# Kernel optimization log

Hardware: AMD Instinct MI355X
Metric: run time of the kernel (lower is better)

Reference implementation:

```python
import jax, jax.numpy as jnp
import numpy as np
import math

B, L, D, H = 2, 2048, 1024, 16
HD = D // H

def setup_inputs() -> dict:
    key = jax.random.key(0)
    ks = jax.random.split(key, 8)
    s = 1.0 / math.sqrt(D)
    # causal additive mask: 0 on/below diagonal, -inf above
    causal = jnp.where(jnp.tril(jnp.ones((L, L), dtype=bool)), 0.0, -jnp.inf)
    causal = causal[None, None].astype(jnp.float32)  # [1,1,L,L]
    return {
        "Q": jax.random.normal(ks[0], (B, L, D), jnp.float32),
        "K": jax.random.normal(ks[1], (B, L, D), jnp.float32),
        "V": jax.random.normal(ks[2], (B, L, D), jnp.float32),
        "attn_mask": causal,
        "padding_mask": jnp.zeros((B, L), dtype=bool),
        "wq": jax.random.normal(ks[3], (D, D), jnp.float32) * s,
        "wk": jax.random.normal(ks[4], (D, D), jnp.float32) * s,
        "wv": jax.random.normal(ks[5], (D, D), jnp.float32) * s,
        "wout": jax.random.normal(ks[6], (D, D), jnp.float32) * s,
    }

def reference(Q, K, V, attn_mask, padding_mask, wq, wk, wv, wout):
    b, l, _ = Q.shape
    # projections (torch Linear: x @ W.T); weights sampled as [out,in]-like square
    def proj(x, w):
        return (x @ w.T).reshape(b, l, H, HD).transpose(0, 2, 1, 3)  # [B,H,L,hd]
    q = proj(Q, wq)
    k = proj(K, wk)
    v = proj(V, wv)
    scores = jnp.einsum("bhqd,bhkd->bhqk", q, k) / math.sqrt(HD)
    scores = scores + attn_mask
    scores = jnp.where(padding_mask[:, None, None, :], -jnp.inf, scores)
    weights = jax.nn.softmax(scores, axis=-1)
    ctx = jnp.einsum("bhqk,bhkd->bhqd", weights, v)
    ctx = ctx.transpose(0, 2, 1, 3).reshape(b, l, D)
    return ctx @ wout.T
```

## Files before the change

### kernel.cpp

```cpp
#include <hip/hip_runtime.h>
#include <stdint.h>
#include <stddef.h>

typedef __bf16 bf16_t;
typedef bf16_t bf16x4 __attribute__((ext_vector_type(4)));
typedef bf16_t bf16x8 __attribute__((ext_vector_type(8)));
typedef float f32x4 __attribute__((ext_vector_type(4)));

#define MFMA_BF16(A_, B_, C_) __builtin_amdgcn_mfma_f32_16x16x32_bf16(A_, B_, C_, 0, 0, 0)

static constexpr int Lseq = 2048;
static constexpr int Dmod = 1024;
static constexpr int Hn   = 16;
static constexpr int HDim = 64;
static constexpr size_t M1 = 1u << 20;

__device__ __forceinline__ int swz(int row, int chunk) {
  return row * 64 + ((chunk ^ (row & 7)) << 3);
}

__device__ __forceinline__ void async_ld16(const bf16_t* g, bf16_t* l) {
  __builtin_amdgcn_global_load_lds(
      (const __attribute__((address_space(1))) void*)g,
      (__attribute__((address_space(3))) void*)l, 16, 0, 0);
}

__global__ __launch_bounds__(256) void cvt_kernel(
    const float* __restrict__ Q, const float* __restrict__ K,
    const float* __restrict__ V, const float* __restrict__ wq,
    const float* __restrict__ wk, const float* __restrict__ wv,
    const float* __restrict__ wout, bf16_t* __restrict__ wsb)
{
  const int s = blockIdx.z;
  const float* __restrict__ src;
  if      (s < 4)   src = Q    + (size_t)s * M1;
  else if (s < 8)   src = K    + (size_t)(s - 4) * M1;
  else if (s < 12)  src = V    + (size_t)(s - 8) * M1;
  else if (s == 12) src = wq;
  else if (s == 13) src = wk;
  else if (s == 14) src = wv;
  else              src = wout;
  bf16_t* __restrict__ dst = wsb + (size_t)s * M1;
  const float scale = (s == 12) ? 0.18033688f : 1.0f;

  const int idx = blockIdx.x * 256 + threadIdx.x;
  float4 a = ((const float4*)src)[idx * 2];
  float4 b = ((const float4*)src)[idx * 2 + 1];
  bf16x8 o;
  o[0] = (bf16_t)(a.x * scale); o[1] = (bf16_t)(a.y * scale);
  o[2] = (bf16_t)(a.z * scale); o[3] = (bf16_t)(a.w * scale);
  o[4] = (bf16_t)(b.x * scale); o[5] = (bf16_t)(b.y * scale);
  o[6] = (bf16_t)(b.z * scale); o[7] = (bf16_t)(b.w * scale);
  ((bf16x8*)dst)[idx] = o;
}

__global__ __launch_bounds__(256) void proj_kernel(
    const bf16_t* __restrict__ Qbf, const bf16_t* __restrict__ Kbf,
    const bf16_t* __restrict__ Vbf, const bf16_t* __restrict__ wqb,
    const bf16_t* __restrict__ wkb, const bf16_t* __restrict__ wvb,
    bf16_t* __restrict__ qo, bf16_t* __restrict__ ko, bf16_t* __restrict__ vo)
{
  const int z = blockIdx.z;
  const bf16_t* __restrict__ A  = (z == 0) ? Qbf : (z == 1) ? Kbf : Vbf;
  const bf16_t* __restrict__ Bw = (z == 0) ? wqb : (z == 1) ? wkb : wvb;
  bf16_t* __restrict__ dst      = (z == 0) ? qo  : (z == 1) ? ko  : vo;

  __shared__ __align__(16) bf16_t As[128 * 64];
  __shared__ __align__(16) bf16_t Bs[64 * 64];

  const int tid  = threadIdx.x;
  const int wave = tid >> 6;
  const int lane = tid & 63;
  const int quad = lane >> 4;
  const int l16  = lane & 15;
  const int wm   = (wave & 1) * 64;
  const int wn   = (wave >> 1) * 32;
  const int m0   = blockIdx.x * 128;
  const int n0   = blockIdx.y * 64;

  const int srow8  = lane >> 3;
  const int schunk = (lane & 7) ^ srow8;

  f32x4 acc[4][2];
#pragma unroll
  for (int i = 0; i < 4; ++i)
#pragma unroll
    for (int j = 0; j < 2; ++j)
#pragma unroll
      for (int e = 0; e < 4; ++e) acc[i][j][e] = 0.0f;

  for (int kt = 0; kt < 16; ++kt) {
    const int k0 = kt * 64;
    __syncthreads();
#pragma unroll
    for (int i = 0; i < 4; ++i) {
      const int rb = wave * 32 + i * 8;
      async_ld16(&A[(size_t)(m0 + rb + srow8) * Dmod + k0 + schunk * 8], &As[rb * 64]);
    }
#pragma unroll
    for (int i = 0; i < 2; ++i) {
      const int rb = wave * 16 + i * 8;
      async_ld16(&Bw[(size_t)(n0 + rb + srow8) * Dmod + k0 + schunk * 8], &Bs[rb * 64]);
    }
    __syncthreads();

    bf16x8 af[4][2], bfr[2][2];
#pragma unroll
    for (int mt = 0; mt < 4; ++mt) {
      const int row = wm + mt * 16 + l16;
      af[mt][0] = *(const bf16x8*)&As[swz(row, quad)];
      af[mt][1] = *(const bf16x8*)&As[swz(row, quad + 4)];
    }
#pragma unroll
    for (int nt = 0; nt < 2; ++nt) {
      const int row = wn + nt * 16 + l16;
      bfr[nt][0] = *(const bf16x8*)&Bs[swz(row, quad)];
      bfr[nt][1] = *(const bf16x8*)&Bs[swz(row, quad + 4)];
    }
#pragma unroll
    for (int mt = 0; mt < 4; ++mt)
#pragma unroll
      for (int nt = 0; nt < 2; ++nt) {
        acc[mt][nt] = MFMA_BF16(af[mt][0], bfr[nt][0], acc[mt][nt]);
        acc[mt][nt] = MFMA_BF16(af[mt][1], bfr[nt][1], acc[mt][nt]);
      }
  }

#pragma unroll
  for (int mt = 0; mt < 4; ++mt) {
    const int grb = m0 + wm + mt * 16 + quad * 4;
    const int bb  = grb >> 11;
    const int lb  = grb & 2047;
#pragma unroll
    for (int nt = 0; nt < 2; ++nt) {
      const int gc = n0 + wn + nt * 16 + l16;
      const int h  = gc >> 6;
      const int hd = gc & 63;
      if (z == 2) {
        bf16x4 pk;
#pragma unroll
        for (int r = 0; r < 4; ++r) pk[r] = (bf16_t)acc[mt][nt][r];
        *(bf16x4*)&dst[(((size_t)(bb * Hn + h) * HDim + hd) << 11) + lb] = pk;
      } else {
#pragma unroll
        for (int r = 0; r < 4; ++r)
          dst[(((size_t)(bb * Hn + h) * Lseq + lb + r) << 6) + hd] = (bf16_t)acc[mt][nt][r];
      }
    }
  }
}

__global__ __launch_bounds__(256) void attn_kernel(
    const bf16_t* __restrict__ q, const bf16_t* __restrict__ k,
    const bf16_t* __restrict__ v, bf16_t* __restrict__ ctx)
{
  const int bh = blockIdx.x;
  const int qt = 31 - blockIdx.y;
  const int bb = bh >> 4;
  const int h  = bh & 15;
  const int q0 = qt * 64;

  const int tid  = threadIdx.x;
  const int wave = tid >> 6;
  const int lane = tid & 63;
  const int quad = lane >> 4;
  const int l16  = lane & 15;

  __shared__ __align__(16) bf16_t Ks[2][64 * 64];
  __shared__ __align__(16) bf16_t Vs[2][64 * 64];
  __shared__ __align__(16) bf16_t Ps[4][16][72];

  const bf16_t* __restrict__ qb = q + (size_t)bh * (Lseq * HDim);
  const bf16_t* __restrict__ kb = k + (size_t)bh * (Lseq * HDim);
  const bf16_t* __restrict__ vb = v + (size_t)bh * (HDim * Lseq);

  const int srow8  = lane >> 3;
  const int schunk = (lane & 7) ^ srow8;

  bf16x8 ones;
#pragma unroll
  for (int i = 0; i < 8; ++i) ones[i] = (bf16_t)1.0f;

  const int qrow = q0 + wave * 16 + l16;
  bf16x8 qf0 = *(const bf16x8*)&qb[(size_t)qrow * HDim + quad * 8];
  bf16x8 qf1 = *(const bf16x8*)&qb[(size_t)qrow * HDim + 32 + quad * 8];

  const bf16_t* ks0 = kb + (size_t)(wave * 16 + srow8) * HDim + schunk * 8;
  const bf16_t* ks1 = ks0 + (size_t)8 * HDim;
  const bf16_t* vs0 = vb + (size_t)(wave * 16 + srow8) * Lseq + schunk * 8;
  const bf16_t* vs1 = vs0 + (size_t)8 * Lseq;
  const int ldo0 = (wave * 16) * 64;
  const int ldo1 = (wave * 16 + 8) * 64;

  int ro0[4], ro1[4];
#pragma unroll
  for (int nt = 0; nt < 4; ++nt) {
    const int row = nt * 16 + l16;
    ro0[nt] = swz(row, quad);
    ro1[nt] = swz(row, quad + 4);
  }

  f32x4 o[4];
  f32x4 lacc;
#pragma unroll
  for (int e = 0; e < 4; ++e) lacc[e] = 0.0f;
#pragma unroll
  for (int nt = 0; nt < 4; ++nt)
#pragma unroll
    for (int e = 0; e < 4; ++e) o[nt][e] = 0.0f;

  async_ld16(ks0, &Ks[0][ldo0]);
  async_ld16(ks1, &Ks[0][ldo1]);
  async_ld16(vs0, &Vs[0][ldo0]);
  async_ld16(vs1, &Vs[0][ldo1]);
  ks0 += (size_t)64 * HDim; ks1 += (size_t)64 * HDim;
  vs0 += 64;                vs1 += 64;

  for (int jt = 0; jt <= qt; ++jt) {
    const int cur = jt & 1;
    __syncthreads();

    if (jt < qt) {
      async_ld16(ks0, &Ks[cur ^ 1][ldo0]);
      async_ld16(ks1, &Ks[cur ^ 1][ldo1]);
      async_ld16(vs0, &Vs[cur ^ 1][ldo0]);
      async_ld16(vs1, &Vs[cur ^ 1][ldo1]);
      ks0 += (size_t)64 * HDim; ks1 += (size_t)64 * HDim;
      vs0 += 64;                vs1 += 64;
    }

    f32x4 s[4];
#pragma unroll
    for (int nt = 0; nt < 4; ++nt) {
#pragma unroll
      for (int e = 0; e < 4; ++e) s[nt][e] = 0.0f;
      bf16x8 kf0 = *(const bf16x8*)&Ks[cur][ro0[nt]];
      bf16x8 kf1 = *(const bf16x8*)&Ks[cur][ro1[nt]];
      s[nt] = MFMA_BF16(kf0, qf0, s[nt]);
      s[nt] = MFMA_BF16(kf1, qf1, s[nt]);
    }

    if (jt == qt) {
#pragma unroll
      for (int nt = 0; nt < 4; ++nt) {
        bf16x4 pk;
#pragma unroll
        for (int r = 0; r < 4; ++r) {
          float val = s[nt][r];
          if (nt * 16 + quad * 4 + r > wave * 16 + l16) val = -1e30f;
          pk[r] = (bf16_t)__builtin_amdgcn_exp2f(val);
        }
        *(bf16x4*)&Ps[wave][l16][nt * 16 + quad * 4] = pk;
      }
    } else {
#pragma unroll
      for (int nt = 0; nt < 4; ++nt) {
        bf16x4 pk;
#pragma unroll
        for (int r = 0; r < 4; ++r)
          pk[r] = (bf16_t)__builtin_amdgcn_exp2f(s[nt][r]);
        *(bf16x4*)&Ps[wave][l16][nt * 16 + quad * 4] = pk;
      }
    }

    bf16x8 pf0 = *(const bf16x8*)&Ps[wave][l16][quad * 8];
    bf16x8 pf1 = *(const bf16x8*)&Ps[wave][l16][32 + quad * 8];

    lacc = MFMA_BF16(pf0, ones, lacc);
    lacc = MFMA_BF16(pf1, ones, lacc);

#pragma unroll
    for (int nt = 0; nt < 4; ++nt) {
      bf16x8 vf0 = *(const bf16x8*)&Vs[cur][ro0[nt]];
      bf16x8 vf1 = *(const bf16x8*)&Vs[cur][ro1[nt]];
      o[nt] = MFMA_BF16(pf0, vf0, o[nt]);
      o[nt] = MFMA_BF16(pf1, vf1, o[nt]);
    }
  }

  float inv[4];
#pragma unroll
  for (int r = 0; r < 4; ++r) inv[r] = 1.0f / lacc[r];
#pragma unroll
  for (int nt = 0; nt < 4; ++nt)
#pragma unroll
    for (int r = 0; r < 4; ++r) {
      const int gq = q0 + wave * 16 + quad * 4 + r;
      ctx[(size_t)(bb * Lseq + gq) * Dmod + h * HDim + nt * 16 + l16] =
          (bf16_t)(o[nt][r] * inv[r]);
    }
}

__global__ __launch_bounds__(256) void out_kernel(
    const bf16_t* __restrict__ Actx, const bf16_t* __restrict__ Bwout,
    float* __restrict__ out)
{
  __shared__ __align__(16) bf16_t As[128 * 64];
  __shared__ __align__(16) bf16_t Bs[64 * 64];

  const int tid  = threadIdx.x;
  const int wave = tid >> 6;
  const int lane = tid & 63;
  const int quad = lane >> 4;
  const int l16  = lane & 15;
  const int wm   = (wave & 1) * 64;
  const int wn   = (wave >> 1) * 32;
  const int m0   = blockIdx.x * 128;
  const int n0   = blockIdx.y * 64;

  const int srow8  = lane >> 3;
  const int schunk = (lane & 7) ^ srow8;

  f32x4 acc[4][2];
#pragma unroll
  for (int i = 0; i < 4; ++i)
#pragma unroll
    for (int j = 0; j < 2; ++j)
#pragma unroll
      for (int e = 0; e < 4; ++e) acc[i][j][e] = 0.0f;

  for (int kt = 0; kt < 16; ++kt) {
    const int k0 = kt * 64;
    __syncthreads();
#pragma unroll
    for (int i = 0; i < 4; ++i) {
      const int rb = wave * 32 + i * 8;
      async_ld16(&Actx[(size_t)(m0 + rb + srow8) * Dmod + k0 + schunk * 8], &As[rb * 64]);
    }
#pragma unroll
    for (int i = 0; i < 2; ++i) {
      const int rb = wave * 16 + i * 8;
      async_ld16(&Bwout[(size_t)(n0 + rb + srow8) * Dmod + k0 + schunk * 8], &Bs[rb * 64]);
    }
    __syncthreads();

    bf16x8 af[4][2], bfr[2][2];
#pragma unroll
    for (int mt = 0; mt < 4; ++mt) {
      const int row = wm + mt * 16 + l16;
      af[mt][0] = *(const bf16x8*)&As[swz(row, quad)];
      af[mt][1] = *(const bf16x8*)&As[swz(row, quad + 4)];
    }
#pragma unroll
    for (int nt = 0; nt < 2; ++nt) {
      const int row = wn + nt * 16 + l16;
      bfr[nt][0] = *(const bf16x8*)&Bs[swz(row, quad)];
      bfr[nt][1] = *(const bf16x8*)&Bs[swz(row, quad + 4)];
    }
#pragma unroll
    for (int mt = 0; mt < 4; ++mt)
#pragma unroll
      for (int nt = 0; nt < 2; ++nt) {
        acc[mt][nt] = MFMA_BF16(af[mt][0], bfr[nt][0], acc[mt][nt]);
        acc[mt][nt] = MFMA_BF16(af[mt][1], bfr[nt][1], acc[mt][nt]);
      }
  }

#pragma unroll
  for (int mt = 0; mt < 4; ++mt) {
    const int grb = m0 + wm + mt * 16 + quad * 4;
#pragma unroll
    for (int nt = 0; nt < 2; ++nt) {
      const int gc = n0 + wn + nt * 16 + l16;
#pragma unroll
      for (int r = 0; r < 4; ++r)
        out[(size_t)(grb + r) * Dmod + gc] = acc[mt][nt][r];
    }
  }
}

extern "C" void kernel_launch(void* const* d_in, const int* in_sizes, int n_in,
                              void* d_out, int out_size, void* d_ws, size_t ws_size,
                              hipStream_t stream) {
  (void)in_sizes; (void)n_in; (void)out_size; (void)ws_size;
  const float* Q    = (const float*)d_in[0];
  const float* K    = (const float*)d_in[1];
  const float* V    = (const float*)d_in[2];
  const float* wq   = (const float*)d_in[5];
  const float* wk   = (const float*)d_in[6];
  const float* wv   = (const float*)d_in[7];
  const float* wout = (const float*)d_in[8];
  float* out = (float*)d_out;

  bf16_t* wsb = (bf16_t*)d_ws;
  bf16_t* Qbf   = wsb;
  bf16_t* Kbf   = wsb + 4 * M1;
  bf16_t* Vbf   = wsb + 8 * M1;
  bf16_t* wqb   = wsb + 12 * M1;
  bf16_t* wkb   = wsb + 13 * M1;
  bf16_t* wvb   = wsb + 14 * M1;
  bf16_t* woutb = wsb + 15 * M1;
  bf16_t* qp    = wsb + 16 * M1;
  bf16_t* kp    = wsb + 20 * M1;
  bf16_t* vp    = wsb + 24 * M1;
  bf16_t* cws   = wsb;

  cvt_kernel<<<dim3(512, 1, 16), 256, 0, stream>>>(Q, K, V, wq, wk, wv, wout, wsb);
  proj_kernel<<<dim3(32, 16, 3), 256, 0, stream>>>(Qbf, Kbf, Vbf, wqb, wkb, wvb, qp, kp, vp);
  attn_kernel<<<dim3(32, 32), 256, 0, stream>>>(qp, kp, vp, cws);
  out_kernel<<<dim3(32, 16), 256, 0, stream>>>(cws, woutb, out);
}
```

Baseline: 212.5 us.

## Double attention query tile to 128 rows per block, two 16-row sub-tiles per wave

Each attention block now covers 128 query rows instead of 64, and each wave handles two 16-row query sub-tiles against the same K/V tile in shared memory. This halves K/V global loads and LDS fragment reads per query row and gives each wave more MFMA work per barrier. A per-wave causal check skips key tiles that lie fully above that wave's rows. Costs are more registers per thread (launch bounds now ask for 2 blocks per CU), half as many blocks, and idle waves in the diagonal tiles, which reduces parallelism and load balance.

```diff
diff --git a/kernel.cpp b/kernel.cpp
--- a/kernel.cpp
+++ b/kernel.cpp
@@ -150,15 +150,15 @@
   }
 }
 
-__global__ __launch_bounds__(256) void attn_kernel(
+__global__ __launch_bounds__(256, 2) void attn_kernel(
     const bf16_t* __restrict__ q, const bf16_t* __restrict__ k,
     const bf16_t* __restrict__ v, bf16_t* __restrict__ ctx)
 {
   const int bh = blockIdx.x;
-  const int qt = 31 - blockIdx.y;
+  const int qt = 15 - blockIdx.y;
   const int bb = bh >> 4;
   const int h  = bh & 15;
-  const int q0 = qt * 64;
+  const int q0 = qt * 128;
 
   const int tid  = threadIdx.x;
   const int wave = tid >> 6;
@@ -168,7 +168,7 @@
 
   __shared__ __align__(16) bf16_t Ks[2][64 * 64];
   __shared__ __align__(16) bf16_t Vs[2][64 * 64];
-  __shared__ __align__(16) bf16_t Ps[4][16][72];
+  __shared__ __align__(16) bf16_t Ps[4][2][16][72];
 
   const bf16_t* __restrict__ qb = q + (size_t)bh * (Lseq * HDim);
   const bf16_t* __restrict__ kb = k + (size_t)bh * (Lseq * HDim);
@@ -181,9 +181,14 @@
 #pragma unroll
   for (int i = 0; i < 8; ++i) ones[i] = (bf16_t)1.0f;
 
-  const int qrow = q0 + wave * 16 + l16;
-  bf16x8 qf0 = *(const bf16x8*)&qb[(size_t)qrow * HDim + quad * 8];
-  bf16x8 qf1 = *(const bf16x8*)&qb[(size_t)qrow * HDim + 32 + quad * 8];
+  const int qlo = q0 + wave * 32;
+  const int qhi = qlo + 31;
+
+  const int qrow0 = qlo + l16;
+  bf16x8 qf00 = *(const bf16x8*)&qb[(size_t)qrow0 * HDim + quad * 8];
+  bf16x8 qf01 = *(const bf16x8*)&qb[(size_t)qrow0 * HDim + 32 + quad * 8];
+  bf16x8 qf10 = *(const bf16x8*)&qb[(size_t)(qrow0 + 16) * HDim + quad * 8];
+  bf16x8 qf11 = *(const bf16x8*)&qb[(size_t)(qrow0 + 16) * HDim + 32 + quad * 8];
 
   const bf16_t* ks0 = kb + (size_t)(wave * 16 + srow8) * HDim + schunk * 8;
   const bf16_t* ks1 = ks0 + (size_t)8 * HDim;
@@ -200,14 +205,14 @@
     ro1[nt] = swz(row, quad + 4);
   }
 
-  f32x4 o[4];
-  f32x4 lacc;
-#pragma unroll
-  for (int e = 0; e < 4; ++e) lacc[e] = 0.0f;
+  f32x4 o0[4], o1[4];
+  f32x4 lacc0, lacc1;
+#pragma unroll
+  for (int e = 0; e < 4; ++e) { lacc0[e] = 0.0f; lacc1[e] = 0.0f; }
 #pragma unroll
   for (int nt = 0; nt < 4; ++nt)
 #pragma unroll
-    for (int e = 0; e < 4; ++e) o[nt][e] = 0.0f;
+    for (int e = 0; e < 4; ++e) { o0[nt][e] = 0.0f; o1[nt][e] = 0.0f; }
 
   async_ld16(ks0, &Ks[0][ldo0]);
   async_ld16(ks1, &Ks[0][ldo1]);
@@ -216,11 +221,12 @@
   ks0 += (size_t)64 * HDim; ks1 += (size_t)64 * HDim;
   vs0 += 64;                vs1 += 64;
 
-  for (int jt = 0; jt <= qt; ++jt) {
+  const int jtmax = 2 * qt + 1;
+  for (int jt = 0; jt <= jtmax; ++jt) {
     const int cur = jt & 1;
     __syncthreads();
 
-    if (jt < qt) {
+    if (jt < jtmax) {
       async_ld16(ks0, &Ks[cur ^ 1][ldo0]);
       async_ld16(ks1, &Ks[cur ^ 1][ldo1]);
       async_ld16(vs0, &Vs[cur ^ 1][ldo0]);
@@ -229,65 +235,96 @@
       vs0 += 64;                vs1 += 64;
     }
 
-    f32x4 s[4];
-#pragma unroll
-    for (int nt = 0; nt < 4; ++nt) {
-#pragma unroll
-      for (int e = 0; e < 4; ++e) s[nt][e] = 0.0f;
-      bf16x8 kf0 = *(const bf16x8*)&Ks[cur][ro0[nt]];
-      bf16x8 kf1 = *(const bf16x8*)&Ks[cur][ro1[nt]];
-      s[nt] = MFMA_BF16(kf0, qf0, s[nt]);
-      s[nt] = MFMA_BF16(kf1, qf1, s[nt]);
-    }
-
-    if (jt == qt) {
+    if (jt * 64 <= qhi) {
+      const bool diag = (jt * 64 + 63 > qlo);
+
+      if (diag) {
+        const int db0 = qlo + l16 - jt * 64;
+        const int db1 = db0 + 16;
+#pragma unroll
+        for (int nt = 0; nt < 4; ++nt) {
+          bf16x8 kf0 = *(const bf16x8*)&Ks[cur][ro0[nt]];
+          bf16x8 kf1 = *(const bf16x8*)&Ks[cur][ro1[nt]];
+          f32x4 s0, s1;
+#pragma unroll
+          for (int e = 0; e < 4; ++e) { s0[e] = 0.0f; s1[e] = 0.0f; }
+          s0 = MFMA_BF16(kf0, qf00, s0);
+          s0 = MFMA_BF16(kf1, qf01, s0);
+          s1 = MFMA_BF16(kf0, qf10, s1);
+          s1 = MFMA_BF16(kf1, qf11, s1);
+          bf16x4 p0, p1;
+#pragma unroll
+          for (int r = 0; r < 4; ++r) {
+            const int kl = nt * 16 + quad * 4 + r;
+            float v0 = (kl > db0) ? -1e30f : s0[r];
+            float v1 = (kl > db1) ? -1e30f : s1[r];
+            p0[r] = (bf16_t)__builtin_amdgcn_exp2f(v0);
+            p1[r] = (bf16_t)__builtin_amdgcn_exp2f(v1);
+          }
+          *(bf16x4*)&Ps[wave][0][l16][nt * 16 + quad * 4] = p0;
+          *(bf16x4*)&Ps[wave][1][l16][nt * 16 + quad * 4] = p1;
+        }
+      } else {
+#pragma unroll
+        for (int nt = 0; nt < 4; ++nt) {
+          bf16x8 kf0 = *(const bf16x8*)&Ks[cur][ro0[nt]];
+          bf16x8 kf1 = *(const bf16x8*)&Ks[cur][ro1[nt]];
+          f32x4 s0, s1;
+#pragma unroll
+          for (int e = 0; e < 4; ++e) { s0[e] = 0.0f; s1[e] = 0.0f; }
+          s0 = MFMA_BF16(kf0, qf00, s0);
+          s0 = MFMA_BF16(kf1, qf01, s0);
+          s1 = MFMA_BF16(kf0, qf10, s1);
+          s1 = MFMA_BF16(kf1, qf11, s1);
+          bf16x4 p0, p1;
+#pragma unroll
+          for (int r = 0; r < 4; ++r) {
+            p0[r] = (bf16_t)__builtin_amdgcn_exp2f(s0[r]);
+            p1[r] = (bf16_t)__builtin_amdgcn_exp2f(s1[r]);
+          }
+          *(bf16x4*)&Ps[wave][0][l16][nt * 16 + quad * 4] = p0;
+          *(bf16x4*)&Ps[wave][1][l16][nt * 16 + quad * 4] = p1;
+        }
+      }
+
+      bf16x8 pf00 = *(const bf16x8*)&Ps[wave][0][l16][quad * 8];
+      bf16x8 pf01 = *(const bf16x8*)&Ps[wave][0][l16][32 + quad * 8];
+      bf16x8 pf10 = *(const bf16x8*)&Ps[wave][1][l16][quad * 8];
+      bf16x8 pf11 = *(const bf16x8*)&Ps[wave][1][l16][32 + quad * 8];
+
+      lacc0 = MFMA_BF16(pf00, ones, lacc0);
+      lacc0 = MFMA_BF16(pf01, ones, lacc0);
+      lacc1 = MFMA_BF16(pf10, ones, lacc1);
+      lacc1 = MFMA_BF16(pf11, ones, lacc1);
+
 #pragma unroll
       for (int nt = 0; nt < 4; ++nt) {
-        bf16x4 pk;
-#pragma unroll
-        for (int r = 0; r < 4; ++r) {
-          float val = s[nt][r];
-          if (nt * 16 + quad * 4 + r > wave * 16 + l16) val = -1e30f;
-          pk[r] = (bf16_t)__builtin_amdgcn_exp2f(val);
-        }
-        *(bf16x4*)&Ps[wave][l16][nt * 16 + quad * 4] = pk;
+        bf16x8 vf0 = *(const bf16x8*)&Vs[cur][ro0[nt]];
+        bf16x8 vf1 = *(const bf16x8*)&Vs[cur][ro1[nt]];
+        o0[nt] = MFMA_BF16(pf00, vf0, o0[nt]);
+        o0[nt] = MFMA_BF16(pf01, vf1, o0[nt]);
+        o1[nt] = MFMA_BF16(pf10, vf0, o1[nt]);
+        o1[nt] = MFMA_BF16(pf11, vf1, o1[nt]);
       }
-    } else {
-#pragma unroll
-      for (int nt = 0; nt < 4; ++nt) {
-        bf16x4 pk;
-#pragma unroll
-        for (int r = 0; r < 4; ++r)
-          pk[r] = (bf16_t)__builtin_amdgcn_exp2f(s[nt][r]);
-        *(bf16x4*)&Ps[wave][l16][nt * 16 + quad * 4] = pk;
-      }
-    }
-
-    bf16x8 pf0 = *(const bf16x8*)&Ps[wave][l16][quad * 8];
-    bf16x8 pf1 = *(const bf16x8*)&Ps[wave][l16][32 + quad * 8];
-
-    lacc = MFMA_BF16(pf0, ones, lacc);
-    lacc = MFMA_BF16(pf1, ones, lacc);
-
-#pragma unroll
-    for (int nt = 0; nt < 4; ++nt) {
-      bf16x8 vf0 = *(const bf16x8*)&Vs[cur][ro0[nt]];
-      bf16x8 vf1 = *(const bf16x8*)&Vs[cur][ro1[nt]];
-      o[nt] = MFMA_BF16(pf0, vf0, o[nt]);
-      o[nt] = MFMA_BF16(pf1, vf1, o[nt]);
-    }
-  }
-
-  float inv[4];
-#pragma unroll
-  for (int r = 0; r < 4; ++r) inv[r] = 1.0f / lacc[r];
+    }
+  }
+
+  float inv0[4], inv1[4];
+#pragma unroll
+  for (int r = 0; r < 4; ++r) {
+    inv0[r] = 1.0f / lacc0[r];
+    inv1[r] = 1.0f / lacc1[r];
+  }
 #pragma unroll
   for (int nt = 0; nt < 4; ++nt)
 #pragma unroll
     for (int r = 0; r < 4; ++r) {
-      const int gq = q0 + wave * 16 + quad * 4 + r;
-      ctx[(size_t)(bb * Lseq + gq) * Dmod + h * HDim + nt * 16 + l16] =
-          (bf16_t)(o[nt][r] * inv[r]);
+      const int gq0 = q0 + wave * 32 + quad * 4 + r;
+      const int gq1 = gq0 + 16;
+      ctx[(size_t)(bb * Lseq + gq0) * Dmod + h * HDim + nt * 16 + l16] =
+          (bf16_t)(o0[nt][r] * inv0[r]);
+      ctx[(size_t)(bb * Lseq + gq1) * Dmod + h * HDim + nt * 16 + l16] =
+          (bf16_t)(o1[nt][r] * inv1[r]);
     }
 }
 
@@ -397,6 +434,6 @@
 
   cvt_kernel<<<dim3(512, 1, 16), 256, 0, stream>>>(Q, K, V, wq, wk, wv, wout, wsb);
   proj_kernel<<<dim3(32, 16, 3), 256, 0, stream>>>(Qbf, Kbf, Vbf, wqb, wkb, wvb, qp, kp, vp);
-  attn_kernel<<<dim3(32, 32), 256, 0, stream>>>(qp, kp, vp, cws);
+  attn_kernel<<<dim3(32, 16), 256, 0, stream>>>(qp, kp, vp, cws);
   out_kernel<<<dim3(32, 16), 256, 0, stream>>>(cws, woutb, out);
 }
```

Result: no change. 209.0 us (-1.6%).

## Load GEMM weight fragments directly to registers; tune attention occupancy and priority

Applied to the files above, without the earlier changes.

In the projection and output GEMMs, the B-operand weight tile is no longer staged through LDS. Each lane loads its MFMA fragment straight from global memory into registers, which removes the Bs buffer and its LDS reads. Weight rows are now read redundantly by the two waves sharing a column slice, and the loads are issued synchronously. The attention kernel also gets a launch-bounds occupancy hint of 3, computes each score tile next to its softmax to shorten register live ranges, and raises wave priority around the PV MFMA block.

```diff
diff --git a/kernel.cpp b/kernel.cpp
--- a/kernel.cpp
+++ b/kernel.cpp
@@ -66,7 +66,6 @@
   bf16_t* __restrict__ dst      = (z == 0) ? qo  : (z == 1) ? ko  : vo;
 
   __shared__ __align__(16) bf16_t As[128 * 64];
-  __shared__ __align__(16) bf16_t Bs[64 * 64];
 
   const int tid  = threadIdx.x;
   const int wave = tid >> 6;
@@ -81,6 +80,8 @@
   const int srow8  = lane >> 3;
   const int schunk = (lane & 7) ^ srow8;
 
+  const bf16_t* __restrict__ bwp = Bw + (size_t)(n0 + wn + l16) * Dmod;
+
   f32x4 acc[4][2];
 #pragma unroll
   for (int i = 0; i < 4; ++i)
@@ -97,25 +98,21 @@
       const int rb = wave * 32 + i * 8;
       async_ld16(&A[(size_t)(m0 + rb + srow8) * Dmod + k0 + schunk * 8], &As[rb * 64]);
     }
-#pragma unroll
-    for (int i = 0; i < 2; ++i) {
-      const int rb = wave * 16 + i * 8;
-      async_ld16(&Bw[(size_t)(n0 + rb + srow8) * Dmod + k0 + schunk * 8], &Bs[rb * 64]);
+
+    bf16x8 bfr[2][2];
+#pragma unroll
+    for (int nt = 0; nt < 2; ++nt) {
+      bfr[nt][0] = *(const bf16x8*)&bwp[(size_t)(nt * 16) * Dmod + k0 + quad * 8];
+      bfr[nt][1] = *(const bf16x8*)&bwp[(size_t)(nt * 16) * Dmod + k0 + 32 + quad * 8];
     }
     __syncthreads();
 
-    bf16x8 af[4][2], bfr[2][2];
+    bf16x8 af[4][2];
 #pragma unroll
     for (int mt = 0; mt < 4; ++mt) {
       const int row = wm + mt * 16 + l16;
       af[mt][0] = *(const bf16x8*)&As[swz(row, quad)];
       af[mt][1] = *(const bf16x8*)&As[swz(row, quad + 4)];
-    }
-#pragma unroll
-    for (int nt = 0; nt < 2; ++nt) {
-      const int row = wn + nt * 16 + l16;
-      bfr[nt][0] = *(const bf16x8*)&Bs[swz(row, quad)];
-      bfr[nt][1] = *(const bf16x8*)&Bs[swz(row, quad + 4)];
     }
 #pragma unroll
     for (int mt = 0; mt < 4; ++mt)
@@ -150,7 +147,7 @@
   }
 }
 
-__global__ __launch_bounds__(256) void attn_kernel(
+__global__ __launch_bounds__(256, 3) void attn_kernel(
     const bf16_t* __restrict__ q, const bf16_t* __restrict__ k,
     const bf16_t* __restrict__ v, bf16_t* __restrict__ ctx)
 {
@@ -181,7 +178,8 @@
 #pragma unroll
   for (int i = 0; i < 8; ++i) ones[i] = (bf16_t)1.0f;
 
-  const int qrow = q0 + wave * 16 + l16;
+  const int qlo = q0 + wave * 16;
+  const int qrow = qlo + l16;
   bf16x8 qf0 = *(const bf16x8*)&qb[(size_t)qrow * HDim + quad * 8];
   bf16x8 qf1 = *(const bf16x8*)&qb[(size_t)qrow * HDim + 32 + quad * 8];
 
@@ -229,25 +227,22 @@
       vs0 += 64;                vs1 += 64;
     }
 
-    f32x4 s[4];
-#pragma unroll
-    for (int nt = 0; nt < 4; ++nt) {
-#pragma unroll
-      for (int e = 0; e < 4; ++e) s[nt][e] = 0.0f;
-      bf16x8 kf0 = *(const bf16x8*)&Ks[cur][ro0[nt]];
-      bf16x8 kf1 = *(const bf16x8*)&Ks[cur][ro1[nt]];
-      s[nt] = MFMA_BF16(kf0, qf0, s[nt]);
-      s[nt] = MFMA_BF16(kf1, qf1, s[nt]);
-    }
-
     if (jt == qt) {
+      const int db = qlo + l16 - jt * 64;
 #pragma unroll
       for (int nt = 0; nt < 4; ++nt) {
+        bf16x8 kf0 = *(const bf16x8*)&Ks[cur][ro0[nt]];
+        bf16x8 kf1 = *(const bf16x8*)&Ks[cur][ro1[nt]];
+        f32x4 s;
+#pragma unroll
+        for (int e = 0; e < 4; ++e) s[e] = 0.0f;
+        s = MFMA_BF16(kf0, qf0, s);
+        s = MFMA_BF16(kf1, qf1, s);
         bf16x4 pk;
 #pragma unroll
         for (int r = 0; r < 4; ++r) {
-          float val = s[nt][r];
-          if (nt * 16 + quad * 4 + r > wave * 16 + l16) val = -1e30f;
+          const int kl = nt * 16 + quad * 4 + r;
+          float val = (kl > db) ? -1e30f : s[r];
           pk[r] = (bf16_t)__builtin_amdgcn_exp2f(val);
         }
         *(bf16x4*)&Ps[wave][l16][nt * 16 + quad * 4] = pk;
@@ -255,16 +250,25 @@
     } else {
 #pragma unroll
       for (int nt = 0; nt < 4; ++nt) {
+        bf16x8 kf0 = *(const bf16x8*)&Ks[cur][ro0[nt]];
+        bf16x8 kf1 = *(const bf16x8*)&Ks[cur][ro1[nt]];
+        f32x4 s;
+#pragma unroll
+        for (int e = 0; e < 4; ++e) s[e] = 0.0f;
+        s = MFMA_BF16(kf0, qf0, s);
+        s = MFMA_BF16(kf1, qf1, s);
         bf16x4 pk;
 #pragma unroll
         for (int r = 0; r < 4; ++r)
-          pk[r] = (bf16_t)__builtin_amdgcn_exp2f(s[nt][r]);
+          pk[r] = (bf16_t)__builtin_amdgcn_exp2f(s[r]);
         *(bf16x4*)&Ps[wave][l16][nt * 16 + quad * 4] = pk;
       }
     }
 
     bf16x8 pf0 = *(const bf16x8*)&Ps[wave][l16][quad * 8];
     bf16x8 pf1 = *(const bf16x8*)&Ps[wave][l16][32 + quad * 8];
+
+    __builtin_amdgcn_s_setprio(1);
 
     lacc = MFMA_BF16(pf0, ones, lacc);
     lacc = MFMA_BF16(pf1, ones, lacc);
@@ -276,6 +280,8 @@
       o[nt] = MFMA_BF16(pf0, vf0, o[nt]);
       o[nt] = MFMA_BF16(pf1, vf1, o[nt]);
     }
+
+    __builtin_amdgcn_s_setprio(0);
   }
 
   float inv[4];
@@ -296,7 +302,6 @@
     float* __restrict__ out)
 {
   __shared__ __align__(16) bf16_t As[128 * 64];
-  __shared__ __align__(16) bf16_t Bs[64 * 64];
 
   const int tid  = threadIdx.x;
   const int wave = tid >> 6;
@@ -311,6 +316,8 @@
   const int srow8  = lane >> 3;
   const int schunk = (lane & 7) ^ srow8;
 
+  const bf16_t* __restrict__ bwp = Bwout + (size_t)(n0 + wn + l16) * Dmod;
+
   f32x4 acc[4][2];
 #pragma unroll
   for (int i = 0; i < 4; ++i)
@@ -327,25 +334,21 @@
       const int rb = wave * 32 + i * 8;
       async_ld16(&Actx[(size_t)(m0 + rb + srow8) * Dmod + k0 + schunk * 8], &As[rb * 64]);
     }
-#pragma unroll
-    for (int i = 0; i < 2; ++i) {
-      const int rb = wave * 16 + i * 8;
-      async_ld16(&Bwout[(size_t)(n0 + rb + srow8) * Dmod + k0 + schunk * 8], &Bs[rb * 64]);
+
+    bf16x8 bfr[2][2];
+#pragma unroll
+    for (int nt = 0; nt < 2; ++nt) {
+      bfr[nt][0] = *(const bf16x8*)&bwp[(size_t)(nt * 16) * Dmod + k0 + quad * 8];
+      bfr[nt][1] = *(const bf16x8*)&bwp[(size_t)(nt * 16) * Dmod + k0 + 32 + quad * 8];
     }
     __syncthreads();
 
-    bf16x8 af[4][2], bfr[2][2];
+    bf16x8 af[4][2];
 #pragma unroll
     for (int mt = 0; mt < 4; ++mt) {
       const int row = wm + mt * 16 + l16;
       af[mt][0] = *(const bf16x8*)&As[swz(row, quad)];
       af[mt][1] = *(const bf16x8*)&As[swz(row, quad + 4)];
-    }
-#pragma unroll
-    for (int nt = 0; nt < 2; ++nt) {
-      const int row = wn + nt * 16 + l16;
-      bfr[nt][0] = *(const bf16x8*)&Bs[swz(row, quad)];
-      bfr[nt][1] = *(const bf16x8*)&Bs[swz(row, quad + 4)];
     }
 #pragma unroll
     for (int mt = 0; mt < 4; ++mt)
```

New measurement: 235.7 us. 11.0% more time.
